# Kernel optimization log

Hardware: AMD Instinct MI355X
Metric: run time of the kernel (lower is better)

The kernel has to match this reference:

```python
import jax, jax.numpy as jnp
import numpy as np

H, CH_IN, DIM, T, V, W = 8, 64, 128, 120, 25, 3
DH = DIM // H
NEG = -9e15

def _pe_spatial(C, T_, V_):
    # spatial positional encoding: position = joint id, repeated over time
    pos = jnp.tile(jnp.arange(V_, dtype=jnp.float32), (T_,))[:, None]          # (T*V,1)
    div = jnp.exp(jnp.arange(0, C, 2, dtype=jnp.float32) * (-np.log(10000.0) / C))
    pe = jnp.zeros((T_ * V_, C), jnp.float32)
    pe = pe.at[:, 0::2].set(jnp.sin(pos * div)).at[:, 1::2].set(jnp.cos(pos * div))
    return pe.reshape(T_, V_, C).transpose(2, 0, 1)[None]                      # (1,C,T,V)

def _unfold3(x):
    # UnfoldTemporalWindows: kernel (3,1), stride 1, pad 1 -> (N,C,T,3*V), window-major u
    N, C, T_, V_ = x.shape
    xp = jnp.pad(x, ((0, 0), (0, 0), (1, 1), (0, 0)))
    win = jnp.stack([xp[:, :, i:i + T_] for i in range(W)], axis=3)            # N C T w V
    return win.reshape(N, C, T_, W * V_)

def _conv1x1(x, Wt, b):
    return jnp.einsum('nctv,dc->ndtv', x, Wt) + b[None, :, None, None]

def _bn(x, g, b, m, v):
    s = (g / jnp.sqrt(v + 1e-5))
    return x * s[None, :, None, None] + (b - m * s)[None, :, None, None]

def setup_inputs():
    key = jax.random.key(0)
    ks = jax.random.split(key, 16)
    N, s = 64, 0.02
    MAXHOP = 5
    x = jax.random.normal(ks[0], (N, CH_IN, T, V), jnp.float32)
    Wq = jax.random.normal(ks[1], (DIM, CH_IN), jnp.float32) * s
    Wk = jax.random.normal(ks[2], (DIM, CH_IN), jnp.float32) * s
    We = jax.random.normal(ks[3], (DIM, CH_IN), jnp.float32) * s
    G = jax.random.uniform(ks[4], (V, V), jnp.float32) * 0.2
    dis_matrix = jax.random.randint(ks[5], (V, V), 0, MAXHOP)
    se_pe = jax.random.normal(ks[6], (MAXHOP, CH_IN), jnp.float32) * s
    dis_graphs = jnp.maximum(jax.random.randint(ks[7], (H, V, V), 0, 2).astype(jnp.float32), jnp.eye(V, dtype=jnp.float32)[None])
    att0 = jnp.tile(jnp.eye(V, dtype=jnp.float32)[None], (H, 1, 1))
    alpha = jax.random.normal(ks[8], (), jnp.float32) * 0.5
    beta = jax.random.normal(ks[9], (), jnp.float32) * 0.5
    Wo = jax.random.normal(ks[10], (DIM, H * CH_IN), jnp.float32) * s
    Wd = jax.random.normal(ks[11], (DIM, CH_IN), jnp.float32) * s
    z, o = jnp.zeros((DIM,), jnp.float32), jnp.ones((DIM,), jnp.float32)
    return dict(x=x, Wq=Wq, bq=z, Wk=Wk, bk=z, We=We, be=z, G=G, se_pe=se_pe,
                att0=att0, alpha=alpha, beta=beta,
                Wo=Wo, b_o=z, g_o=o, be_o=z, m_o=z, v_o=o,
                Wd=Wd, b_d=z, g_d=o, be_d=z, m_d=z, v_d=o,
                dis_matrix=dis_matrix, dis_graphs=dis_graphs)

def reference(x, Wq, bq, Wk, bk, We, be, G, se_pe, att0, alpha, beta,
              Wo, b_o, g_o, be_o, m_o, v_o, Wd, b_d, g_d, be_d, m_d, v_d,
              dis_matrix, dis_graphs):
    N = x.shape[0]
    # spatial PE + structural-encoding gather bias
    y = x + _pe_spatial(CH_IN, T, V)
    y = y + jnp.einsum('nctu,uvc->nctv', x, se_pe[dis_matrix])
    # K on raw joints, Q on temporally-unfolded windows
    k = _conv1x1(y, Wk, bk).reshape(N, H, DH, T, V)
    q = _conv1x1(_unfold3(y), Wq, bq).reshape(N, H, DH, T, W * V)
    att = jnp.einsum('nhctu,nhctv->nhuv', q, k) / (DH * T)
    # hypergraph partition embedding bias
    e = _conv1x1(y, We, be)
    e = jnp.einsum('ndtv,vu->ndtu', e, G).reshape(N, H, DH, T, V)
    att = att + beta * (jnp.einsum('nhctu,nhctv->nhuv', q, e) / (DH * T))
    # per-head distance-graph sparsity mask (tiled over the 3 temporal windows)
    mask = jnp.tile(dis_graphs, (1, W, 1)) > 0                                  # (H,3V,V)
    att = jnp.where(mask[None], att, NEG)
    att = jax.nn.softmax(att, axis=-2)
    # learnable identity bias
    att = att * alpha + jnp.tile(att0, (1, W, 1))[None]
    # aggregate unfolded features
    xs = jnp.einsum('nhuv,nctu->nhctv', att, _unfold3(x)).reshape(N, H * CH_IN, T, V)
    out = _bn(_conv1x1(xs, Wo, b_o), g_o, be_o, m_o, v_o)
    res = _bn(_conv1x1(x, Wd, b_d), g_d, be_d, m_d, v_d)
    return jax.nn.leaky_relu(res + out, 0.1)
```

## Files before the change

### kernel.cpp

```cpp
#include <hip/hip_runtime.h>
#include <hip/hip_bf16.h>
#include <math.h>

#define NB   64
#define CIN  64
#define DIMD 128
#define TT   120
#define VV   25
#define HH   8
#define DHD  16
#define WW   3
#define UU   75
#define TC2  12
#define TCO8 8

typedef __hip_bfloat16 bf16;
typedef float        f32x4  __attribute__((ext_vector_type(4)));
typedef unsigned int u32x4  __attribute__((ext_vector_type(4)));
typedef unsigned int u32x2  __attribute__((ext_vector_type(2)));
typedef __bf16       bf16x8 __attribute__((ext_vector_type(8)));

__device__ __forceinline__ float b2f(bf16 v)  { return __bfloat162float(v); }
__device__ __forceinline__ bf16  f2b(float v) { return __float2bfloat16(v); }

__device__ __forceinline__ unsigned short f2bu(float f) {
  unsigned u = __builtin_bit_cast(unsigned, f);
  return (unsigned short)((u + 0x7fffu + ((u >> 16) & 1u)) >> 16);
}
__device__ __forceinline__ float bfu(unsigned short s) {
  unsigned u = ((unsigned)s) << 16;
  return __builtin_bit_cast(float, u);
}
__device__ __forceinline__ unsigned pack2(float a, float b) {
  return ((unsigned)f2bu(b) << 16) | (unsigned)f2bu(a);
}

__device__ __forceinline__ f32x4 mfma_bf16(u32x4 a, u32x4 b, f32x4 d) {
  return __builtin_amdgcn_mfma_f32_16x16x32_bf16(
      __builtin_bit_cast(bf16x8, a), __builtin_bit_cast(bf16x8, b), d, 0, 0, 0);
}

#define PRIO_HI() __builtin_amdgcn_s_setprio(1)
#define PRIO_LO() __builtin_amdgcn_s_setprio(0)

__global__ __launch_bounds__(256) void k_pack_w(
    const float* __restrict__ Wo, const float* __restrict__ g_o,
    const float* __restrict__ v_o,
    const float* __restrict__ Wd, const float* __restrict__ g_d,
    const float* __restrict__ v_d,
    const float* __restrict__ Wq, const float* __restrict__ Wk,
    const float* __restrict__ We, const float* __restrict__ beta,
    unsigned short* __restrict__ woF, unsigned short* __restrict__ wdF,
    unsigned short* __restrict__ wqF, unsigned short* __restrict__ wkF,
    unsigned short* __restrict__ weF)
{
  const int i = blockIdx.x * 256 + threadIdx.x;
  if (i < 65536) {
    const int j = i & 7, d = (i >> 3) & 127, kg = (i >> 10) & 3;
    const int ks = (i >> 12) & 1, h = (i >> 13) & 7;
    const float sc = g_o[d] * rsqrtf(v_o[d] + 1e-5f);
    woF[i] = f2bu(sc * Wo[d * 512 + h * 64 + ks * 32 + kg * 8 + j]);
  } else {
    const int r = i - 65536;
    const int which = r >> 13;
    const int l = r & 8191;
    const int j = l & 7, d = (l >> 3) & 127, kg = (l >> 10) & 3;
    const int ks = (l >> 12) & 1;
    const int c = ks * 32 + kg * 8 + j;
    if (which == 0) {
      const float sc = g_d[d] * rsqrtf(v_d[d] + 1e-5f);
      wdF[l] = f2bu(sc * Wd[d * 64 + c]);
    } else if (which == 1) {
      wqF[l] = f2bu(Wq[d * 64 + c]);
    } else if (which == 2) {
      wkF[l] = f2bu(Wk[d * 64 + c]);
    } else {
      weF[l] = f2bu(beta[0] * We[d * 64 + c]);
    }
  }
}

__global__ __launch_bounds__(256, 3) void k_qke_mfma9(
    const float* __restrict__ x,
    const unsigned short* __restrict__ wqF, const float* __restrict__ bq,
    const unsigned short* __restrict__ wkF, const float* __restrict__ bk,
    const unsigned short* __restrict__ weF, const float* __restrict__ be,
    const float* __restrict__ G,  const float* __restrict__ beta,
    const float* __restrict__ se_pe, const int* __restrict__ dis,
    bf16* __restrict__ qy, bf16* __restrict__ kkp)
{
  const int n = blockIdx.x / 30, t0 = (blockIdx.x % 30) * 4;
  __shared__ alignas(16) char uA[16384];
  __shared__ alignas(16) char yCM[16384];
  __shared__ alignas(16) unsigned short yT[112][64];
  __shared__ alignas(16) unsigned short GlT[32][32];
  __shared__ alignas(16) float spl[5][64];
  __shared__ alignas(16) float gsum[32];
  __shared__ alignas(16) float biasb[384];

  unsigned short* xf  = (unsigned short*)uA;
  char*           yTG = uA;
  unsigned short* MhT = (unsigned short*)yCM;
  char*           yC  = yCM;

  const int tid = threadIdx.x;
  {
    const float* xb = x + (size_t)n * 192000 + t0 * 25;
    for (int i = tid; i < 8192; i += 256) {
      const int u = i & 31, r = i >> 5;
      const int c = r >> 2, t = r & 3;
      xf[i] = (u < VV) ? f2bu(xb[c * 3000 + t * 25 + u]) : 0;
    }
  }
  for (int i = tid; i < 5120; i += 256) {
    const int hop = i / 1024, r = i % 1024, v = r >> 5, u = r & 31;
    MhT[i] = (u < VV && v < VV && dis[u * 25 + v] == hop) ? 0x3f80 : 0;
  }
  for (int i = tid; i < 320; i += 256) spl[i / 64][i % 64] = se_pe[i];
  for (int i = tid; i < 1024; i += 256) {
    const int v = i >> 5, u = i & 31;
    const float g = (v < 25 && u < 25) ? G[u * 25 + v] : 0.f;
    *(unsigned short*)((char*)GlT + v * 64 + ((u * 2) ^ ((v & 7) << 4))) =
        f2bu(g);
  }
  if (tid < 25) {
    float s = 0.f;
    for (int u = 0; u < 25; ++u) s += G[u * 25 + tid];
    gsum[tid] = s;
  }
  for (int i = tid; i < 384; i += 256)
    biasb[i] = (i < 128) ? bq[i] : (i < 256 ? bk[i - 128] : be[i - 256]);
  for (int i = tid; i < 12 * 64; i += 256)
    yT[100 + (i >> 6)][i & 63] = 0;
  __syncthreads();

  const int lane = tid & 63, wid = tid >> 6;
  const int m16 = lane & 15, kg = lane >> 4;

  #define LOAD_PFRAGS(af, Fsrc)                                                \
    _Pragma("unroll")                                                          \
    for (int mt = 0; mt < 2; ++mt) {                                           \
      const int d_ = wid * 32 + mt * 16 + m16;                                 \
      _Pragma("unroll")                                                        \
      for (int ks = 0; ks < 2; ++ks)                                           \
        af[mt][ks] = *(const u32x4*)((Fsrc) +                                  \
                      (((ks * 4 + kg) * 128 + d_) << 3));                      \
    }

  {
    u32x4 bh[2][5];
    #pragma unroll
    for (int ntv = 0; ntv < 2; ++ntv)
      #pragma unroll
      for (int hop = 0; hop < 5; ++hop)
        bh[ntv][hop] = *(const u32x4*)&MhT[hop * 1024 +
                                          (ntv * 16 + m16) * 32 + kg * 8];
    __syncthreads();

    #pragma unroll
    for (int mt4 = 0; mt4 < 4; ++mt4) {
      const int r0 = (wid * 4 + mt4) * 16;
      const u32x4 a = *(const u32x4*)&xf[(r0 + m16) * 32 + kg * 8];
      const int c = (r0 + kg * 4) >> 2;
      float spc[5];
      #pragma unroll
      for (int hop = 0; hop < 5; ++hop) spc[hop] = spl[hop][c];
      const float dv = expf(-(float)(c & ~1) * (logf(10000.0f) / 64.0f));
      #pragma unroll
      for (int ntv = 0; ntv < 2; ++ntv) {
        f32x4 zh[5];
        PRIO_HI();
        #pragma unroll
        for (int hop = 0; hop < 5; ++hop) {
          zh[hop] = (f32x4)0.f;
          zh[hop] = mfma_bf16(a, bh[ntv][hop], zh[hop]);
        }
        PRIO_LO();
        const int v = ntv * 16 + m16;
        if (v < VV) {
          const float pe = (c & 1) ? cosf((float)v * dv) : sinf((float)v * dv);
          #pragma unroll
          for (int i = 0; i < 4; ++i) {
            const int r = r0 + kg * 4 + i;
            float yv = bfu(xf[r * 32 + v]) + pe;
            #pragma unroll
            for (int hop = 0; hop < 5; ++hop)
              yv = fmaf(spc[hop], zh[hop][i], yv);
            const unsigned short yb = f2bu(yv);
            const int tv = i * 25 + v;
            *(unsigned short*)((char*)yT + tv * 128 +
                               ((c * 2) ^ ((tv & 7) << 4))) = yb;
            *(unsigned short*)(yC + (i * 64 + c) * 64 +
                               ((v * 2) ^ ((c & 7) << 4))) = yb;
          }
        } else {
          #pragma unroll
          for (int i = 0; i < 4; ++i) {
            const int c2 = c;
            *(unsigned short*)(yC + (i * 64 + c2) * 64 +
                               ((v * 2) ^ ((c2 & 7) << 4))) = 0;
          }
        }
      }
    }
  }
  __syncthreads();

  for (int i = tid; i < 12 * 64; i += 256)
    *(unsigned short*)(yTG + (100 + (i >> 6)) * 128 + ((i & 63) * 2)) = 0;
  {
    const int t = wid;
    u32x4 bg[2];
    #pragma unroll
    for (int ntv = 0; ntv < 2; ++ntv) {
      const int v = ntv * 16 + m16;
      bg[ntv] = *(const u32x4*)((const char*)GlT + v * 64 +
                                ((kg * 16) ^ ((v & 7) << 4)));
    }
    #pragma unroll
    for (int mtile = 0; mtile < 4; ++mtile) {
      const int cr = mtile * 16 + m16;
      const u32x4 a = *(const u32x4*)(yC + (t * 64 + cr) * 64 +
                                      ((kg * 16) ^ ((cr & 7) << 4)));
      #pragma unroll
      for (int ntv = 0; ntv < 2; ++ntv) {
        f32x4 d = (f32x4)0.f;
        d = mfma_bf16(a, bg[ntv], d);
        const int v = ntv * 16 + m16;
        if (v < 25) {
          const int tv = t * 25 + v;
          #pragma unroll
          for (int i = 0; i < 4; ++i) {
            const int cc = mtile * 16 + kg * 4 + i;
            *(unsigned short*)(yTG + tv * 128 + ((cc * 2) ^ ((tv & 7) << 4))) =
                f2bu(d[i]);
          }
        }
      }
    }
  }
  __syncthreads();

  bf16* qyb = qy  + (size_t)n * 384000 + t0 * 25;
  bf16* kkb = kkp + (size_t)n * 384000 + t0 * 25;
  const float betav = beta[0];

  {
    u32x4 aq[2][2];
    LOAD_PFRAGS(aq, wqF);
    for (int nt = 0; nt < 7; ++nt) {
      const int tv = nt * 16 + m16;
      const u32x4 b0 = *(const u32x4*)((const char*)yT + tv * 128 +
                        (((kg * 8) * 2) ^ ((tv & 7) << 4)));
      const u32x4 b1 = *(const u32x4*)((const char*)yT + tv * 128 +
                        (((32 + kg * 8) * 2) ^ ((tv & 7) << 4)));
      PRIO_HI();
      f32x4 acc0 = (f32x4)0.f, acc1 = (f32x4)0.f;
      acc0 = mfma_bf16(aq[0][0], b0, acc0);
      acc0 = mfma_bf16(aq[0][1], b1, acc0);
      acc1 = mfma_bf16(aq[1][0], b0, acc1);
      acc1 = mfma_bf16(aq[1][1], b1, acc1);
      PRIO_LO();
      if (tv < 100) {
        #pragma unroll
        for (int mt = 0; mt < 2; ++mt) {
          const f32x4 acc = mt ? acc1 : acc0;
          const int dr = wid * 32 + mt * 16 + kg * 4;
          #pragma unroll
          for (int i2 = 0; i2 < 4; ++i2)
            qyb[(size_t)(dr + i2) * 3000 + tv] = f2b(acc[i2] + biasb[dr + i2]);
        }
      }
    }
  }

  f32x4 kacc[2][7];
  #pragma unroll
  for (int mt = 0; mt < 2; ++mt)
    #pragma unroll
    for (int nt = 0; nt < 7; ++nt) kacc[mt][nt] = (f32x4)0.f;
  {
    u32x4 ak[2][2];
    LOAD_PFRAGS(ak, wkF);
    for (int nt = 0; nt < 7; ++nt) {
      const int tv = nt * 16 + m16;
      const u32x4 b0 = *(const u32x4*)((const char*)yT + tv * 128 +
                        (((kg * 8) * 2) ^ ((tv & 7) << 4)));
      const u32x4 b1 = *(const u32x4*)((const char*)yT + tv * 128 +
                        (((32 + kg * 8) * 2) ^ ((tv & 7) << 4)));
      PRIO_HI();
      #pragma unroll
      for (int mt = 0; mt < 2; ++mt) {
        kacc[mt][nt] = mfma_bf16(ak[mt][0], b0, kacc[mt][nt]);
        kacc[mt][nt] = mfma_bf16(ak[mt][1], b1, kacc[mt][nt]);
      }
      PRIO_LO();
    }
  }

  {
    u32x4 ae[2][2];
    LOAD_PFRAGS(ae, weF);
    for (int nt = 0; nt < 7; ++nt) {
      const int tv = nt * 16 + m16;
      const u32x4 b0 = *(const u32x4*)(yTG + tv * 128 +
                        (((kg * 8) * 2) ^ ((tv & 7) << 4)));
      const u32x4 b1 = *(const u32x4*)(yTG + tv * 128 +
                        (((32 + kg * 8) * 2) ^ ((tv & 7) << 4)));
      PRIO_HI();
      #pragma unroll
      for (int mt = 0; mt < 2; ++mt) {
        kacc[mt][nt] = mfma_bf16(ae[mt][0], b0, kacc[mt][nt]);
        kacc[mt][nt] = mfma_bf16(ae[mt][1], b1, kacc[mt][nt]);
      }
      PRIO_LO();
      if (tv < 100) {
        const int vv = tv % 25;
        #pragma unroll
        for (int mt = 0; mt < 2; ++mt) {
          const int dr = wid * 32 + mt * 16 + kg * 4;
          #pragma unroll
          for (int i2 = 0; i2 < 4; ++i2)
            kkb[(size_t)(dr + i2) * 3000 + tv] =
                f2b(kacc[mt][nt][i2] + biasb[128 + dr + i2] +
                    betav * biasb[256 + dr + i2] * gsum[vv]);
        }
      }
    }
  }
  #undef LOAD_PFRAGS
}

__global__ __launch_bounds__(256) void k_att_mfma(
    const bf16* __restrict__ qy, const bf16* __restrict__ kkp,
    const float* __restrict__ bq, const float* __restrict__ disg,
    const float* __restrict__ att0, const float* __restrict__ alpha,
    unsigned short* __restrict__ attP)
{
  const int n = blockIdx.x / HH, h = blockIdx.x % HH;
  __shared__ alignas(16) unsigned short qsA[80][200];
  __shared__ alignas(16) unsigned short ksB[32][200];
  __shared__ alignas(16) float att_s[80][28];
  __shared__ float mxv[32], smv[32];
  const int tid = threadIdx.x;
  const int lane = tid & 63, wid = tid >> 6;
  const int m16 = lane & 15, kg = lane >> 4;

  const unsigned short* qyb =
      (const unsigned short*)(qy + ((size_t)(n * DIMD + h * DHD)) * TT * VV);
  const unsigned short* kkb =
      (const unsigned short*)(kkp + ((size_t)(n * DIMD + h * DHD)) * TT * VV);

  f32x4 acc[3];
  #pragma unroll
  for (int s = 0; s < 3; ++s) acc[s] = (f32x4)0.f;

  for (int c = 0; c < 10; ++c) {
    const int t0 = c * TC2;
    __syncthreads();
    for (int it = tid; it < 416; it += 256) {
      if (it < 224) {
        const int dh = it / 14, j = it % 14, tq = t0 + j - 1;
        unsigned short vals[25];
        if (tq >= 0 && tq < TT) {
          const unsigned short* src = qyb + ((size_t)dh * TT + tq) * VV;
          #pragma unroll
          for (int u = 0; u < 25; ++u) vals[u] = src[u];
        } else {
          const unsigned short bqv = f2bu(bq[h * DHD + dh]);
          #pragma unroll
          for (int u = 0; u < 25; ++u) vals[u] = bqv;
        }
        #pragma unroll
        for (int w = 0; w < 3; ++w) {
          const int tt = tq - t0 - w + 1;
          if (tt >= 0 && tt < TC2) {
            const int col = tt * 16 + dh;
            #pragma unroll
            for (int u = 0; u < 25; ++u) qsA[w * 25 + u][col] = vals[u];
          }
        }
      } else {
        const int r = it - 224, dh = r / TC2, tt = r % TC2;
        const unsigned short* src = kkb + ((size_t)dh * TT + t0 + tt) * VV;
        const int col = tt * 16 + dh;
        #pragma unroll
        for (int v = 0; v < 25; ++v) ksB[v][col] = src[v];
      }
    }
    __syncthreads();
    PRIO_HI();
    #pragma unroll
    for (int s = 0; s < 3; ++s) {
      const int tidx = wid + 4 * s;
      if (tidx < 10) {
        const int mtile = tidx >> 1, ntile = tidx & 1;
        #pragma unroll
        for (int ks = 0; ks < 6; ++ks) {
          const u32x4 a = *(const u32x4*)&qsA[mtile * 16 + m16][ks * 32 + kg * 8];
          const u32x4 b = *(const u32x4*)&ksB[ntile * 16 + m16][ks * 32 + kg * 8];
          acc[s] = mfma_bf16(a, b, acc[s]);
        }
      }
    }
    PRIO_LO();
  }
  __syncthreads();
  #pragma unroll
  for (int s = 0; s < 3; ++s) {
    const int tidx = wid + 4 * s;
    if (tidx < 10) {
      const int mtile = tidx >> 1, ntile = tidx & 1;
      const int v = ntile * 16 + m16;
      if (v < VV) {
        #pragma unroll
        for (int i = 0; i < 4; ++i)
          att_s[mtile * 16 + kg * 4 + i][v] = acc[s][i];
      }
    }
  }
  __syncthreads();
  const float inv = 1.0f / (float)(DHD * TT);
  for (int i = tid; i < UU * VV; i += 256) {
    const int u = i / VV, v = i % VV;
    const bool m = disg[(h * VV + u % VV) * VV + v] > 0.f;
    att_s[u][v] = m ? att_s[u][v] * inv : -9e15f;
  }
  __syncthreads();
  if (tid < VV) {
    float mx = -INFINITY;
    for (int u = 0; u < UU; ++u) mx = fmaxf(mx, att_s[u][tid]);
    float sm = 0.f;
    for (int u = 0; u < UU; ++u) sm += expf(att_s[u][tid] - mx);
    mxv[tid] = mx; smv[tid] = sm;
  }
  __syncthreads();
  const float al = alpha[0];
  unsigned* dst = (unsigned*)(attP + ((size_t)(n * HH + h) * 32) * 104);
  for (int i = tid; i < 1664; i += 256) {
    const int vc = i / 52, u0 = (i % 52) * 2;
    unsigned val = 0u;
    if (vc < VV) {
      float f0 = 0.f, f1 = 0.f;
      if (u0 < UU)
        f0 = expf(att_s[u0][vc] - mxv[vc]) / smv[vc] * al
             + att0[(h * VV + u0 % VV) * VV + vc];
      if (u0 + 1 < UU)
        f1 = expf(att_s[u0 + 1][vc] - mxv[vc]) / smv[vc] * al
             + att0[(h * VV + (u0 + 1) % VV) * VV + vc];
      val = pack2(f0, f1);
    }
    dst[i] = val;
  }
}

__global__ __launch_bounds__(512) void k_out_mfma7(
    const float* __restrict__ x, const unsigned short* __restrict__ attP,
    const unsigned short* __restrict__ woF, const unsigned short* __restrict__ wdF,
    const float* __restrict__ b_o,
    const float* __restrict__ g_o, const float* __restrict__ be_o,
    const float* __restrict__ m_o, const float* __restrict__ v_o,
    const float* __restrict__ b_d,
    const float* __restrict__ g_d, const float* __restrict__ be_d,
    const float* __restrict__ m_d, const float* __restrict__ v_d,
    float* __restrict__ out)
{
  const int n = blockIdx.x / 15, t0 = (blockIdx.x % 15) * TCO8;
  __shared__ alignas(16) char uB[54272];
  __shared__ alignas(16) unsigned short attB[2][32][104];
  unsigned short* xu4 = (unsigned short*)uB;
  const int tid = threadIdx.x;
  const int lane = tid & 63, wid = tid >> 6;
  const int m16 = lane & 15, kg = lane >> 4;

  #define XSLB(b) (uB + (b) * 27136)

  #define STAGE_XU4(tb)                                                        \
    for (int i = tid; i < 4 * 64 * 48; i += 512) {                             \
      const int u0 = (i % 48) * 2, c = (i / 48) & 63, tr = i / (48 * 64);      \
      float f0 = 0.f, f1 = 0.f;                                                \
      if (u0 < UU) {                                                           \
        const int w = u0 / VV, up = u0 % VV, ts = t0 + (tb) + tr + w - 1;      \
        if (ts >= 0 && ts < TT) f0 = x[((n * 64 + c) * TT + ts) * VV + up];    \
      }                                                                        \
      if (u0 + 1 < UU) {                                                       \
        const int u = u0 + 1, w = u / VV, up = u % VV;                         \
        const int ts = t0 + (tb) + tr + w - 1;                                 \
        if (ts >= 0 && ts < TT) f1 = x[((n * 64 + c) * TT + ts) * VV + up];    \
      }                                                                        \
      *(unsigned*)(xu4 + (tr * 64 + c) * 104 + u0) = pack2(f0, f1);            \
    }

  #define STAGE_ATT(hh, buf)                                                   \
    {                                                                          \
      const u32x4* srcv =                                                      \
          (const u32x4*)(attP + ((size_t)(n * HH + (hh)) * 32) * 104);         \
      u32x4* dstv = (u32x4*)&attB[buf][0][0];                                  \
      for (int i = tid; i < 416; i += 512) dstv[i] = srcv[i];                  \
    }

  STAGE_XU4(0);
  __syncthreads();
  u32x4 af[4][3];
  if (wid < 4) {
    #pragma unroll
    for (int mt = 0; mt < 4; ++mt)
      #pragma unroll
      for (int ks = 0; ks < 3; ++ks)
        af[mt][ks] = *(const u32x4*)(xu4 + (wid * 64 + mt * 16 + m16) * 104 +
                                     ks * 32 + kg * 8);
  }
  __syncthreads();
  STAGE_XU4(4);
  STAGE_ATT(0, 0);
  __syncthreads();
  if (wid >= 4) {
    #pragma unroll
    for (int mt = 0; mt < 4; ++mt)
      #pragma unroll
      for (int ks = 0; ks < 3; ++ks)
        af[mt][ks] = *(const u32x4*)(xu4 + ((wid - 4) * 64 + mt * 16 + m16) * 104 +
                                     ks * 32 + kg * 8);
  }
  __syncthreads();
  for (int i = tid; i < 2 * 12 * 64; i += 512) {
    const int b = i / (12 * 64), r = i % (12 * 64);
    *(unsigned short*)(XSLB(b) + (200 + (r >> 6)) * 128 + ((r & 63) * 2)) = 0;
  }

  const int th = wid >> 2, dq = wid & 3;

  f32x4 acc2[2][7];
  #pragma unroll
  for (int mt = 0; mt < 2; ++mt)
    #pragma unroll
    for (int nt = 0; nt < 7; ++nt) acc2[mt][nt] = (f32x4)0.f;

  for (int h = 0; h <= HH; ++h) {
    const int pb = h & 1;
    char* xs = XSLB(pb);
    u32x4 a2[2][2];
    #pragma unroll
    for (int mt = 0; mt < 2; ++mt) {
      const int d = dq * 32 + mt * 16 + m16;
      #pragma unroll
      for (int ks = 0; ks < 2; ++ks) {
        const unsigned short* src = (h < HH)
            ? (woF + ((((h * 2 + ks) * 4 + kg) * 128 + d) << 3))
            : (wdF + ((((ks) * 4 + kg) * 128 + d) << 3));
        a2[mt][ks] = *(const u32x4*)src;
      }
    }
    if (h + 1 < HH) { STAGE_ATT(h + 1, (h + 1) & 1); }
    f32x4 a1[4][2];
    if (h < HH) {
      u32x4 bfr[2][3];
      #pragma unroll
      for (int nt = 0; nt < 2; ++nt)
        #pragma unroll
        for (int ks = 0; ks < 3; ++ks)
          bfr[nt][ks] =
              *(const u32x4*)&attB[pb][nt * 16 + m16][ks * 32 + kg * 8];
      PRIO_HI();
      #pragma unroll
      for (int mt = 0; mt < 4; ++mt)
        #pragma unroll
        for (int nt = 0; nt < 2; ++nt) {
          a1[mt][nt] = (f32x4)0.f;
          #pragma unroll
          for (int ks = 0; ks < 3; ++ks)
            a1[mt][nt] = mfma_bf16(af[mt][ks], bfr[nt][ks], a1[mt][nt]);
        }
      PRIO_LO();
    }
    if (h < HH) {
      #pragma unroll
      for (int mt = 0; mt < 4; ++mt)
        #pragma unroll
        for (int nt = 0; nt < 2; ++nt) {
          const int v = nt * 16 + m16;
          if (v < VV) {
            const int tv = wid * VV + v;
            const int c0 = mt * 16 + kg * 4;
            u32x2 pk;
            pk[0] = pack2(a1[mt][nt][0], a1[mt][nt][1]);
            pk[1] = pack2(a1[mt][nt][2], a1[mt][nt][3]);
            char* p = xs + tv * 128 + ((c0 * 2) ^ ((tv & 7) << 4));
            *(u32x2*)p = pk;
          }
        }
    } else {
      for (int i = tid; i < 12800; i += 512) {
        const int c = i / 200, j = i % 200;
        const float f = x[((size_t)(n * 64 + c) * TT + t0 + j / 25) * VV + j % 25];
        *(unsigned short*)(xs + j * 128 + ((c * 2) ^ ((j & 7) << 4))) =
            f2bu(f);
      }
    }
    __syncthreads();
    PRIO_HI();
    #pragma unroll
    for (int nt = 0; nt < 7; ++nt) {
      const int tv = th * 100 + nt * 16 + m16;
      const u32x4 b0 = *(const u32x4*)(xs + tv * 128 +
                        (((kg * 8) * 2) ^ ((tv & 7) << 4)));
      const u32x4 b1 = *(const u32x4*)(xs + tv * 128 +
                        (((32 + kg * 8) * 2) ^ ((tv & 7) << 4)));
      #pragma unroll
      for (int mt = 0; mt < 2; ++mt) {
        acc2[mt][nt] = mfma_bf16(a2[mt][0], b0, acc2[mt][nt]);
        acc2[mt][nt] = mfma_bf16(a2[mt][1], b1, acc2[mt][nt]);
      }
    }
    PRIO_LO();
  }

  #pragma unroll
  for (int mt = 0; mt < 2; ++mt) {
    float cc[4];
    #pragma unroll
    for (int i = 0; i < 4; ++i) {
      const int d = dq * 32 + mt * 16 + kg * 4 + i;
      const float so2 = g_o[d] * rsqrtf(v_o[d] + 1e-5f);
      const float sd2 = g_d[d] * rsqrtf(v_d[d] + 1e-5f);
      cc[i] = b_o[d] * so2 + be_o[d] - m_o[d] * so2
            + b_d[d] * sd2 + be_d[d] - m_d[d] * sd2;
    }
    #pragma unroll
    for (int nt = 0; nt < 7; ++nt) {
      const int tvl = nt * 16 + m16;
      if (tvl < 100) {
        const int tv = th * 100 + tvl;
        const int t = t0 + tv / VV, v = tv % VV;
        #pragma unroll
        for (int i = 0; i < 4; ++i) {
          const int d = dq * 32 + mt * 16 + kg * 4 + i;
          const float z = acc2[mt][nt][i] + cc[i];
          out[((n * DIMD + d) * TT + t) * VV + v] = (z >= 0.f) ? z : 0.1f * z;
        }
      }
    }
  }
  #undef STAGE_XU4
  #undef STAGE_ATT
  #undef XSLB
}

extern "C" void kernel_launch(void* const* d_in, const int* in_sizes, int n_in,
                              void* d_out, int out_size, void* d_ws, size_t ws_size,
                              hipStream_t stream)
{
  (void)in_sizes; (void)n_in; (void)out_size; (void)ws_size;
  const float* x     = (const float*)d_in[0];
  const float* Wq    = (const float*)d_in[1];
  const float* bq    = (const float*)d_in[2];
  const float* Wk    = (const float*)d_in[3];
  const float* bk    = (const float*)d_in[4];
  const float* We    = (const float*)d_in[5];
  const float* be    = (const float*)d_in[6];
  const float* G     = (const float*)d_in[7];
  const float* sepe  = (const float*)d_in[8];
  const float* att0  = (const float*)d_in[9];
  const float* alpha = (const float*)d_in[10];
  const float* beta  = (const float*)d_in[11];
  const float* Wo    = (const float*)d_in[12];
  const float* b_o   = (const float*)d_in[13];
  const float* g_o   = (const float*)d_in[14];
  const float* be_o  = (const float*)d_in[15];
  const float* m_o   = (const float*)d_in[16];
  const float* v_o   = (const float*)d_in[17];
  const float* Wd    = (const float*)d_in[18];
  const float* b_d   = (const float*)d_in[19];
  const float* g_d   = (const float*)d_in[20];
  const float* be_d  = (const float*)d_in[21];
  const float* m_d   = (const float*)d_in[22];
  const float* v_d   = (const float*)d_in[23];
  const int*   dism  = (const int*)d_in[24];
  const float* disg  = (const float*)d_in[25];

  char* ws = (char*)d_ws;
  bf16* qy   = (bf16*)(ws);
  bf16* kkp  = (bf16*)(ws + 49152000);
  unsigned short* attP = (unsigned short*)(ws + 98304000);
  unsigned short* woF  = (unsigned short*)(ws + 101711872);
  unsigned short* wdF  = (unsigned short*)(ws + 101842944);
  unsigned short* wqF  = (unsigned short*)(ws + 101859328);
  unsigned short* wkF  = (unsigned short*)(ws + 101875712);
  unsigned short* weF  = (unsigned short*)(ws + 101892096);

  k_pack_w<<<384, 256, 0, stream>>>(Wo, g_o, v_o, Wd, g_d, v_d,
                                    Wq, Wk, We, beta,
                                    woF, wdF, wqF, wkF, weF);
  k_qke_mfma9<<<NB * 30, 256, 0, stream>>>(x, wqF, bq, wkF, bk, weF, be,
                                           G, beta, sepe, dism, qy, kkp);
  k_att_mfma<<<NB * HH, 256, 0, stream>>>(qy, kkp, bq, disg, att0, alpha, attP);
  k_out_mfma7<<<NB * 15, 512, 0, stream>>>(x, attP, woF, wdF,
                                           b_o, g_o, be_o, m_o, v_o,
                                           b_d, g_d, be_d, m_d, v_d,
                                           (float*)d_out);
}
```

Before: 319.4 us.

## Restructure output kernel to per-wave timesteps with private LDS and no block barriers

The output-projection kernel moves from 512-thread blocks covering 8 timesteps to 256-thread blocks covering 4 timesteps, doubling the grid. Each wave now owns one timestep end to end: it computes the attention-weighted features into a private LDS slice and immediately runs the Wo/Wd projection over all 128 output channels, so the per-head __syncthreads and the shared attention double-buffer go away. Attention and weight fragments are read straight from global memory inside the loop rather than staged in LDS. In exchange, weights are re-read per wave, the accumulator array grows to 8x2 tiles, and latency hiding now rests on occupancy instead of explicit staging.

Result: slower. 418.5 us (+31.0%).

```diff
diff --git a/kernel.cpp b/kernel.cpp
--- a/kernel.cpp
+++ b/kernel.cpp
@@ -12,7 +12,6 @@
 #define WW   3
 #define UU   75
 #define TC2  12
-#define TCO8 8
 
 typedef __hip_bfloat16 bf16;
 typedef float        f32x4  __attribute__((ext_vector_type(4)));
@@ -454,7 +453,7 @@
   }
 }
 
-__global__ __launch_bounds__(512) void k_out_mfma7(
+__global__ __launch_bounds__(256) void k_out_mfma8(
     const float* __restrict__ x, const unsigned short* __restrict__ attP,
     const unsigned short* __restrict__ woF, const unsigned short* __restrict__ wdF,
     const float* __restrict__ b_o,
@@ -465,102 +464,63 @@
     const float* __restrict__ m_d, const float* __restrict__ v_d,
     float* __restrict__ out)
 {
-  const int n = blockIdx.x / 15, t0 = (blockIdx.x % 15) * TCO8;
-  __shared__ alignas(16) char uB[54272];
-  __shared__ alignas(16) unsigned short attB[2][32][104];
+  const int n = blockIdx.x / 30, t0 = (blockIdx.x % 30) * 4;
+  __shared__ alignas(16) char uB[53248];
   unsigned short* xu4 = (unsigned short*)uB;
   const int tid = threadIdx.x;
   const int lane = tid & 63, wid = tid >> 6;
   const int m16 = lane & 15, kg = lane >> 4;
 
-  #define XSLB(b) (uB + (b) * 27136)
-
-  #define STAGE_XU4(tb)                                                        \
-    for (int i = tid; i < 4 * 64 * 48; i += 512) {                             \
-      const int u0 = (i % 48) * 2, c = (i / 48) & 63, tr = i / (48 * 64);      \
-      float f0 = 0.f, f1 = 0.f;                                                \
-      if (u0 < UU) {                                                           \
-        const int w = u0 / VV, up = u0 % VV, ts = t0 + (tb) + tr + w - 1;      \
-        if (ts >= 0 && ts < TT) f0 = x[((n * 64 + c) * TT + ts) * VV + up];    \
-      }                                                                        \
-      if (u0 + 1 < UU) {                                                       \
-        const int u = u0 + 1, w = u / VV, up = u % VV;                         \
-        const int ts = t0 + (tb) + tr + w - 1;                                 \
-        if (ts >= 0 && ts < TT) f1 = x[((n * 64 + c) * TT + ts) * VV + up];    \
-      }                                                                        \
-      *(unsigned*)(xu4 + (tr * 64 + c) * 104 + u0) = pack2(f0, f1);            \
-    }
-
-  #define STAGE_ATT(hh, buf)                                                   \
-    {                                                                          \
-      const u32x4* srcv =                                                      \
-          (const u32x4*)(attP + ((size_t)(n * HH + (hh)) * 32) * 104);         \
-      u32x4* dstv = (u32x4*)&attB[buf][0][0];                                  \
-      for (int i = tid; i < 416; i += 512) dstv[i] = srcv[i];                  \
-    }
-
-  STAGE_XU4(0);
+  for (int i = tid; i < 4 * 64 * 48; i += 256) {
+    const int u0 = (i % 48) * 2, c = (i / 48) & 63, tr = i / (48 * 64);
+    float f0 = 0.f, f1 = 0.f;
+    if (u0 < UU) {
+      const int w = u0 / VV, up = u0 % VV, ts = t0 + tr + w - 1;
+      if (ts >= 0 && ts < TT) f0 = x[((n * 64 + c) * TT + ts) * VV + up];
+    }
+    if (u0 + 1 < UU) {
+      const int u = u0 + 1, w = u / VV, up = u % VV;
+      const int ts = t0 + tr + w - 1;
+      if (ts >= 0 && ts < TT) f1 = x[((n * 64 + c) * TT + ts) * VV + up];
+    }
+    *(unsigned*)(xu4 + (tr * 64 + c) * 104 + u0) = pack2(f0, f1);
+  }
   __syncthreads();
   u32x4 af[4][3];
-  if (wid < 4) {
-    #pragma unroll
-    for (int mt = 0; mt < 4; ++mt)
-      #pragma unroll
-      for (int ks = 0; ks < 3; ++ks)
-        af[mt][ks] = *(const u32x4*)(xu4 + (wid * 64 + mt * 16 + m16) * 104 +
-                                     ks * 32 + kg * 8);
-  }
-  __syncthreads();
-  STAGE_XU4(4);
-  STAGE_ATT(0, 0);
-  __syncthreads();
-  if (wid >= 4) {
-    #pragma unroll
-    for (int mt = 0; mt < 4; ++mt)
-      #pragma unroll
-      for (int ks = 0; ks < 3; ++ks)
-        af[mt][ks] = *(const u32x4*)(xu4 + ((wid - 4) * 64 + mt * 16 + m16) * 104 +
-                                     ks * 32 + kg * 8);
-  }
-  __syncthreads();
-  for (int i = tid; i < 2 * 12 * 64; i += 512) {
-    const int b = i / (12 * 64), r = i % (12 * 64);
-    *(unsigned short*)(XSLB(b) + (200 + (r >> 6)) * 128 + ((r & 63) * 2)) = 0;
-  }
-
-  const int th = wid >> 2, dq = wid & 3;
-
-  f32x4 acc2[2][7];
   #pragma unroll
-  for (int mt = 0; mt < 2; ++mt)
-    #pragma unroll
-    for (int nt = 0; nt < 7; ++nt) acc2[mt][nt] = (f32x4)0.f;
+  for (int mt = 0; mt < 4; ++mt)
+    #pragma unroll
+    for (int ks = 0; ks < 3; ++ks)
+      af[mt][ks] = *(const u32x4*)(xu4 + (wid * 64 + mt * 16 + m16) * 104 +
+                                   ks * 32 + kg * 8);
+  __syncthreads();
+
+  char* xs = uB + wid * 4096;
+  for (int j = lane; j < 7 * 64; j += 64) {
+    const int v = 25 + j / 64 + 0;
+    const int c = j % 64;
+    *(unsigned short*)(xs + (25 + (j >> 6)) * 128 + ((c * 2) ^ (((25 + (j >> 6)) & 7) << 4))) = 0;
+    (void)v;
+  }
+
+  const unsigned short* attn = attP + (size_t)n * HH * 32 * 104;
+
+  f32x4 acc[8][2];
+  #pragma unroll
+  for (int mt = 0; mt < 8; ++mt)
+    #pragma unroll
+    for (int nt = 0; nt < 2; ++nt) acc[mt][nt] = (f32x4)0.f;
 
   for (int h = 0; h <= HH; ++h) {
-    const int pb = h & 1;
-    char* xs = XSLB(pb);
-    u32x4 a2[2][2];
-    #pragma unroll
-    for (int mt = 0; mt < 2; ++mt) {
-      const int d = dq * 32 + mt * 16 + m16;
-      #pragma unroll
-      for (int ks = 0; ks < 2; ++ks) {
-        const unsigned short* src = (h < HH)
-            ? (woF + ((((h * 2 + ks) * 4 + kg) * 128 + d) << 3))
-            : (wdF + ((((ks) * 4 + kg) * 128 + d) << 3));
-        a2[mt][ks] = *(const u32x4*)src;
-      }
-    }
-    if (h + 1 < HH) { STAGE_ATT(h + 1, (h + 1) & 1); }
-    f32x4 a1[4][2];
     if (h < HH) {
       u32x4 bfr[2][3];
       #pragma unroll
       for (int nt = 0; nt < 2; ++nt)
         #pragma unroll
         for (int ks = 0; ks < 3; ++ks)
-          bfr[nt][ks] =
-              *(const u32x4*)&attB[pb][nt * 16 + m16][ks * 32 + kg * 8];
+          bfr[nt][ks] = *(const u32x4*)(attn + ((size_t)h * 32 +
+                          (nt * 16 + m16)) * 104 + ks * 32 + kg * 8);
+      f32x4 a1[4][2];
       PRIO_HI();
       #pragma unroll
       for (int mt = 0; mt < 4; ++mt)
@@ -572,78 +532,78 @@
             a1[mt][nt] = mfma_bf16(af[mt][ks], bfr[nt][ks], a1[mt][nt]);
         }
       PRIO_LO();
-    }
-    if (h < HH) {
       #pragma unroll
       for (int mt = 0; mt < 4; ++mt)
         #pragma unroll
         for (int nt = 0; nt < 2; ++nt) {
           const int v = nt * 16 + m16;
           if (v < VV) {
-            const int tv = wid * VV + v;
             const int c0 = mt * 16 + kg * 4;
             u32x2 pk;
             pk[0] = pack2(a1[mt][nt][0], a1[mt][nt][1]);
             pk[1] = pack2(a1[mt][nt][2], a1[mt][nt][3]);
-            char* p = xs + tv * 128 + ((c0 * 2) ^ ((tv & 7) << 4));
-            *(u32x2*)p = pk;
+            *(u32x2*)(xs + v * 128 + ((c0 * 2) ^ ((v & 7) << 4))) = pk;
           }
         }
     } else {
-      for (int i = tid; i < 12800; i += 512) {
-        const int c = i / 200, j = i % 200;
-        const float f = x[((size_t)(n * 64 + c) * TT + t0 + j / 25) * VV + j % 25];
-        *(unsigned short*)(xs + j * 128 + ((c * 2) ^ ((j & 7) << 4))) =
-            f2bu(f);
-      }
-    }
-    __syncthreads();
-    PRIO_HI();
-    #pragma unroll
-    for (int nt = 0; nt < 7; ++nt) {
-      const int tv = th * 100 + nt * 16 + m16;
-      const u32x4 b0 = *(const u32x4*)(xs + tv * 128 +
-                        (((kg * 8) * 2) ^ ((tv & 7) << 4)));
-      const u32x4 b1 = *(const u32x4*)(xs + tv * 128 +
-                        (((32 + kg * 8) * 2) ^ ((tv & 7) << 4)));
-      #pragma unroll
-      for (int mt = 0; mt < 2; ++mt) {
-        acc2[mt][nt] = mfma_bf16(a2[mt][0], b0, acc2[mt][nt]);
-        acc2[mt][nt] = mfma_bf16(a2[mt][1], b1, acc2[mt][nt]);
-      }
-    }
-    PRIO_LO();
-  }
-
+      const int t = t0 + wid;
+      for (int j = lane; j < 1600; j += 64) {
+        const int c = j / 25, v = j % 25;
+        const float f = x[((size_t)(n * 64 + c) * TT + t) * VV + v];
+        *(unsigned short*)(xs + v * 128 + ((c * 2) ^ ((v & 7) << 4))) = f2bu(f);
+      }
+    }
+    #pragma unroll
+    for (int nt = 0; nt < 2; ++nt) {
+      const int v = nt * 16 + m16;
+      const u32x4 b0 = *(const u32x4*)(xs + v * 128 +
+                        (((kg * 8) * 2) ^ ((v & 7) << 4)));
+      const u32x4 b1 = *(const u32x4*)(xs + v * 128 +
+                        (((32 + kg * 8) * 2) ^ ((v & 7) << 4)));
+      PRIO_HI();
+      #pragma unroll
+      for (int mt = 0; mt < 8; ++mt) {
+        const int d = mt * 16 + m16;
+        u32x4 a20, a21;
+        if (h < HH) {
+          a20 = *(const u32x4*)(woF + ((((h * 2 + 0) * 4 + kg) * 128 + d) << 3));
+          a21 = *(const u32x4*)(woF + ((((h * 2 + 1) * 4 + kg) * 128 + d) << 3));
+        } else {
+          a20 = *(const u32x4*)(wdF + ((((0) * 4 + kg) * 128 + d) << 3));
+          a21 = *(const u32x4*)(wdF + ((((1) * 4 + kg) * 128 + d) << 3));
+        }
+        acc[mt][nt] = mfma_bf16(a20, b0, acc[mt][nt]);
+        acc[mt][nt] = mfma_bf16(a21, b1, acc[mt][nt]);
+      }
+      PRIO_LO();
+    }
+  }
+
+  const int t = t0 + wid;
   #pragma unroll
-  for (int mt = 0; mt < 2; ++mt) {
+  for (int mt = 0; mt < 8; ++mt) {
     float cc[4];
     #pragma unroll
     for (int i = 0; i < 4; ++i) {
-      const int d = dq * 32 + mt * 16 + kg * 4 + i;
+      const int d = mt * 16 + kg * 4 + i;
       const float so2 = g_o[d] * rsqrtf(v_o[d] + 1e-5f);
       const float sd2 = g_d[d] * rsqrtf(v_d[d] + 1e-5f);
       cc[i] = b_o[d] * so2 + be_o[d] - m_o[d] * so2
             + b_d[d] * sd2 + be_d[d] - m_d[d] * sd2;
     }
     #pragma unroll
-    for (int nt = 0; nt < 7; ++nt) {
-      const int tvl = nt * 16 + m16;
-      if (tvl < 100) {
-        const int tv = th * 100 + tvl;
-        const int t = t0 + tv / VV, v = tv % VV;
+    for (int nt = 0; nt < 2; ++nt) {
+      const int v = nt * 16 + m16;
+      if (v < VV) {
         #pragma unroll
         for (int i = 0; i < 4; ++i) {
-          const int d = dq * 32 + mt * 16 + kg * 4 + i;
-          const float z = acc2[mt][nt][i] + cc[i];
+          const int d = mt * 16 + kg * 4 + i;
+          const float z = acc[mt][nt][i] + cc[i];
           out[((n * DIMD + d) * TT + t) * VV + v] = (z >= 0.f) ? z : 0.1f * z;
         }
       }
     }
   }
-  #undef STAGE_XU4
-  #undef STAGE_ATT
-  #undef XSLB
 }
 
 extern "C" void kernel_launch(void* const* d_in, const int* in_sizes, int n_in,
@@ -694,7 +654,7 @@
   k_qke_mfma9<<<NB * 30, 256, 0, stream>>>(x, wqF, bq, wkF, bk, weF, be,
                                            G, beta, sepe, dism, qy, kkp);
   k_att_mfma<<<NB * HH, 256, 0, stream>>>(qy, kkp, bq, disg, att0, alpha, attP);
-  k_out_mfma7<<<NB * 15, 512, 0, stream>>>(x, attP, woF, wdF,
+  k_out_mfma8<<<NB * 30, 256, 0, stream>>>(x, attP, woF, wdF,
                                            b_o, g_o, be_o, m_o, v_o,
                                            b_d, g_d, be_d, m_d, v_d,
                                            (float*)d_out);
```
